# Kernel tuning notes

Measured on AMD Instinct MI355X. Metric: run time of the kernel, lower is better.

The kernel has to match this reference:

```python
import jax, jax.numpy as jnp
import numpy as np

N = 4096
DIM_IN = 512
DIM_Q = 128
DIM_K = 128
NUM_GRAPHS = 16
NODES_PER_GRAPH = N // NUM_GRAPHS
NEG = -1000000.0


def setup_inputs() -> dict:
    key = jax.random.key(0)
    ks = jax.random.split(key, 10)
    x = jax.random.normal(ks[0], (N, DIM_IN), dtype=jnp.float32)
    b = jax.random.normal(ks[1], (N, N), dtype=jnp.float32)
    c = jax.random.normal(ks[2], (N, N), dtype=jnp.float32)
    sparse_mask = jax.random.randint(ks[3], (N, N), 0, 2).astype(jnp.int32)
    ptr = (jnp.arange(NUM_GRAPHS + 1) * NODES_PER_GRAPH).astype(jnp.int32)
    # linear layer params (q, k, v): y = x @ W.T + bias
    Wq = jax.random.normal(ks[4], (DIM_Q, DIM_IN), dtype=jnp.float32) * 0.02
    bq = jnp.zeros((DIM_Q,), dtype=jnp.float32)
    Wk = jax.random.normal(ks[5], (DIM_K, DIM_IN), dtype=jnp.float32) * 0.02
    bk = jnp.zeros((DIM_K,), dtype=jnp.float32)
    Wv = jax.random.normal(ks[6], (DIM_K, DIM_IN), dtype=jnp.float32) * 0.02
    bv = jnp.zeros((DIM_K,), dtype=jnp.float32)
    return {"x": x, "b": b, "c": c, "ptr": ptr, "sparse_mask": sparse_mask,
            "Wq": Wq, "bq": bq, "Wk": Wk, "bk": bk, "Wv": Wv, "bv": bv}


def reference(x, b, c, ptr, sparse_mask, Wq, bq, Wk, bk, Wv, bv):
    n = x.shape[0]
    q = x @ Wq.T + bq            # [N, dq]
    k = x @ Wk.T + bk            # [N, dk]
    v = x @ Wv.T + bv            # [N, dk]
    # graph id per node from ptr; block-diagonal (same-graph) mask
    gid = jnp.searchsorted(ptr, jnp.arange(n), side='right') - 1
    block = gid[:, None] == gid[None, :]                       # [N, N] bool
    scale = q.shape[-1] ** 0.5
    # compute_a: QK^T/sqrt(dq) on the block diagonal, zeros elsewhere
    a = jnp.where(block, (q @ k.T) / scale, 0.0)
    a = a + b + c
    keep = block & (sparse_mask != 0)
    a = jnp.where(keep, a, NEG)
    sm = jax.nn.softmax(a, axis=-1) * keep.astype(x.dtype)
    return sm @ v
```

## Files before the change

### kernel.cpp

```cpp
#include <hip/hip_runtime.h>
#include <hip/hip_bf16.h>

#define N_NODES 4096
#define DIM_IN 512
#define DIM_QK 128
#define BLK 256
#define NUM_G 16
#define NEGV -1000000.0f

typedef __bf16 bf16x8 __attribute__((ext_vector_type(8)));
typedef float  f32x4  __attribute__((ext_vector_type(4)));

__global__ __launch_bounds__(256) void cvt_kernel(
    const float* __restrict__ x,
    const float* __restrict__ Wq, const float* __restrict__ Wk,
    const float* __restrict__ Wv,
    __bf16* __restrict__ xb, __bf16* __restrict__ wb)
{
    const int i = blockIdx.x * 256 + threadIdx.x;
    if (i < 524288) {
        const float4 v = ((const float4*)x)[i];
        __bf16* o = xb + i * 4;
        o[0] = (__bf16)v.x; o[1] = (__bf16)v.y;
        o[2] = (__bf16)v.z; o[3] = (__bf16)v.w;
    } else {
        const int j = i - 524288;
        if (j < 49152) {
            const int m = j / 16384;
            const float* W = (m == 0) ? Wq : (m == 1 ? Wk : Wv);
            const float4 v = ((const float4*)W)[j - m * 16384];
            __bf16* o = wb + j * 4;
            o[0] = (__bf16)v.x; o[1] = (__bf16)v.y;
            o[2] = (__bf16)v.z; o[3] = (__bf16)v.w;
        }
    }
}

__global__ __launch_bounds__(128) void qkv_mfma(
    const __bf16* __restrict__ xb, const __bf16* __restrict__ wb,
    const float* __restrict__ bq, const float* __restrict__ bk,
    const float* __restrict__ bv,
    __bf16* __restrict__ qb, __bf16* __restrict__ kb, __bf16* __restrict__ vtb)
{
    const int mat    = blockIdx.y >> 1;
    const int colOff = (blockIdx.y & 1) * 64;
    const int wave = threadIdx.x >> 6;
    const int lane = threadIdx.x & 63;
    const int lr   = lane & 15;
    const int quad = lane >> 4;
    const int row0 = blockIdx.x * 32 + wave * 16;

    const __bf16* W    = wb + mat * (DIM_QK * DIM_IN);
    const float*  bias = (mat == 0) ? bq : (mat == 1 ? bk : bv);

    f32x4 acc[4];
    #pragma unroll
    for (int i = 0; i < 4; ++i) acc[i] = (f32x4){0.f, 0.f, 0.f, 0.f};

    const __bf16* arow = xb + (size_t)(row0 + lr) * DIM_IN + quad * 8;
    const __bf16* brow = W + (size_t)(colOff + lr) * DIM_IN + quad * 8;

    #pragma unroll 4
    for (int kt = 0; kt < 16; ++kt) {
        const bf16x8 a = *(const bf16x8*)(arow + kt * 32);
        #pragma unroll
        for (int nt = 0; nt < 4; ++nt) {
            const bf16x8 b = *(const bf16x8*)(brow + nt * 16 * DIM_IN + kt * 32);
            acc[nt] = __builtin_amdgcn_mfma_f32_16x16x32_bf16(a, b, acc[nt], 0, 0, 0);
        }
    }

    #pragma unroll
    for (int nt = 0; nt < 4; ++nt) {
        const int col = colOff + nt * 16 + lr;
        const float bs = bias[col];
        #pragma unroll
        for (int r = 0; r < 4; ++r) {
            const int row = row0 + quad * 4 + r;
            const __bf16 o = (__bf16)(acc[nt][r] + bs);
            if (mat == 0)      qb[(size_t)row * DIM_QK + col] = o;
            else if (mat == 1) kb[(size_t)row * DIM_QK + col] = o;
            else               vtb[(size_t)col * N_NODES + row] = o;
        }
    }
}

#define PSTR 272

__global__ __launch_bounds__(256, 1) void attn_mfma(
    const float* __restrict__ bmat, const float* __restrict__ cmat,
    const int* __restrict__ mask,
    const __bf16* __restrict__ qb, const __bf16* __restrict__ kb,
    const __bf16* __restrict__ vtb,
    float* __restrict__ out)
{
    __shared__ __bf16 plds[16 * PSTR];
    __shared__ float redm[4][16];
    __shared__ float reds[4][16];

    const int tid  = threadIdx.x;
    const int w    = tid >> 6;
    const int lane = tid & 63;
    const int lr   = lane & 15;
    const int quad = lane >> 4;
    const int g    = blockIdx.x >> 4;
    const int tile = blockIdx.x & 15;
    const int row0 = g * BLK + tile * 16;
    const int col0 = g * BLK;

    bf16x8 aq[4];
    #pragma unroll
    for (int kt = 0; kt < 4; ++kt)
        aq[kt] = *(const bf16x8*)(qb + (size_t)(row0 + lr) * DIM_QK + kt * 32 + quad * 8);

    bf16x8 bk[16];
    #pragma unroll
    for (int kt = 0; kt < 4; ++kt)
        #pragma unroll
        for (int nt = 0; nt < 4; ++nt)
            bk[kt * 4 + nt] = *(const bf16x8*)(kb
                + (size_t)(col0 + w * 64 + nt * 16 + lr) * DIM_QK + kt * 32 + quad * 8);

    bf16x8 bv[16];
    #pragma unroll
    for (int nt2 = 0; nt2 < 2; ++nt2)
        #pragma unroll
        for (int kt = 0; kt < 8; ++kt)
            bv[nt2 * 8 + kt] = *(const bf16x8*)(vtb
                + (size_t)(w * 32 + nt2 * 16 + lr) * N_NODES + col0 + kt * 32 + quad * 8);

    float bbv[16], ccv[16];
    int   mmv[16];
    #pragma unroll
    for (int nt = 0; nt < 4; ++nt)
        #pragma unroll
        for (int r = 0; r < 4; ++r) {
            const size_t idx = (size_t)(row0 + quad * 4 + r) * N_NODES
                             + col0 + w * 64 + nt * 16 + lr;
            bbv[nt * 4 + r] = bmat[idx];
            ccv[nt * 4 + r] = cmat[idx];
            mmv[nt * 4 + r] = mask[idx];
        }

    f32x4 s[4];
    #pragma unroll
    for (int nt = 0; nt < 4; ++nt) s[nt] = (f32x4){0.f, 0.f, 0.f, 0.f};

    #pragma unroll
    for (int kt = 0; kt < 4; ++kt)
        #pragma unroll
        for (int nt = 0; nt < 4; ++nt)
            s[nt] = __builtin_amdgcn_mfma_f32_16x16x32_bf16(aq[kt], bk[kt * 4 + nt],
                                                            s[nt], 0, 0, 0);

    const float rscale = 0.08838834764831845f;
    #pragma unroll
    for (int nt = 0; nt < 4; ++nt)
        #pragma unroll
        for (int r = 0; r < 4; ++r) {
            const int i = nt * 4 + r;
            s[nt][r] = mmv[i] ? (s[nt][r] * rscale + bbv[i] + ccv[i]) : NEGV;
        }

    float mr[4] = {-3e38f, -3e38f, -3e38f, -3e38f};
    #pragma unroll
    for (int nt = 0; nt < 4; ++nt)
        #pragma unroll
        for (int r = 0; r < 4; ++r) mr[r] = fmaxf(mr[r], s[nt][r]);
    #pragma unroll
    for (int off = 1; off <= 8; off <<= 1)
        #pragma unroll
        for (int r = 0; r < 4; ++r) mr[r] = fmaxf(mr[r], __shfl_xor(mr[r], off));
    if (lr == 0) {
        #pragma unroll
        for (int r = 0; r < 4; ++r) redm[w][quad * 4 + r] = mr[r];
    }
    __syncthreads();
    float M[4];
    #pragma unroll
    for (int r = 0; r < 4; ++r) {
        const int rw = quad * 4 + r;
        M[r] = fmaxf(fmaxf(redm[0][rw], redm[1][rw]), fmaxf(redm[2][rw], redm[3][rw]));
    }

    float sum[4] = {0.f, 0.f, 0.f, 0.f};
    #pragma unroll
    for (int nt = 0; nt < 4; ++nt)
        #pragma unroll
        for (int r = 0; r < 4; ++r) {
            const float e = (s[nt][r] > -1e5f) ? __expf(s[nt][r] - M[r]) : 0.f;
            s[nt][r] = e;
            sum[r] += e;
        }
    #pragma unroll
    for (int off = 1; off <= 8; off <<= 1)
        #pragma unroll
        for (int r = 0; r < 4; ++r) sum[r] += __shfl_xor(sum[r], off);
    if (lr == 0) {
        #pragma unroll
        for (int r = 0; r < 4; ++r) reds[w][quad * 4 + r] = sum[r];
    }
    __syncthreads();
    float inv[4];
    #pragma unroll
    for (int r = 0; r < 4; ++r) {
        const int rw = quad * 4 + r;
        const float t = reds[0][rw] + reds[1][rw] + reds[2][rw] + reds[3][rw];
        inv[r] = (t > 0.f) ? (1.f / t) : 0.f;
    }

    #pragma unroll
    for (int nt = 0; nt < 4; ++nt)
        #pragma unroll
        for (int r = 0; r < 4; ++r)
            plds[(quad * 4 + r) * PSTR + w * 64 + nt * 16 + lr] =
                (__bf16)(s[nt][r] * inv[r]);
    __syncthreads();

    #pragma unroll
    for (int nt2 = 0; nt2 < 2; ++nt2) {
        f32x4 o = (f32x4){0.f, 0.f, 0.f, 0.f};
        #pragma unroll
        for (int kt = 0; kt < 8; ++kt) {
            const bf16x8 a = *(const bf16x8*)(plds + lr * PSTR + kt * 32 + quad * 8);
            o = __builtin_amdgcn_mfma_f32_16x16x32_bf16(a, bv[nt2 * 8 + kt], o, 0, 0, 0);
        }
        #pragma unroll
        for (int r = 0; r < 4; ++r)
            out[(size_t)(row0 + quad * 4 + r) * DIM_QK + w * 32 + nt2 * 16 + lr] = o[r];
    }
}

extern "C" void kernel_launch(void* const* d_in, const int* in_sizes, int n_in,
                              void* d_out, int out_size, void* d_ws, size_t ws_size,
                              hipStream_t stream) {
    const float* x    = (const float*)d_in[0];
    const float* bmat = (const float*)d_in[1];
    const float* cmat = (const float*)d_in[2];
    const int*   mask = (const int*)d_in[4];
    const float* Wq   = (const float*)d_in[5];
    const float* bq   = (const float*)d_in[6];
    const float* Wk   = (const float*)d_in[7];
    const float* bk   = (const float*)d_in[8];
    const float* Wv   = (const float*)d_in[9];
    const float* bv   = (const float*)d_in[10];
    float* out = (float*)d_out;

    __bf16* xb  = (__bf16*)d_ws;
    __bf16* wb  = xb + (size_t)N_NODES * DIM_IN;
    __bf16* qb  = wb + 3 * DIM_QK * DIM_IN;
    __bf16* kb  = qb + (size_t)N_NODES * DIM_QK;
    __bf16* vtb = kb + (size_t)N_NODES * DIM_QK;

    cvt_kernel<<<dim3((524288 + 49152 + 255) / 256), 256, 0, stream>>>(
        x, Wq, Wk, Wv, xb, wb);

    qkv_mfma<<<dim3(128, 6), 128, 0, stream>>>(
        xb, wb, bq, bk, bv, qb, kb, vtb);

    attn_mfma<<<dim3(NUM_G * 16), 256, 0, stream>>>(
        bmat, cmat, mask, qb, kb, vtb, out);
}
```

Measured before the change: 196.4 us.

## Fuse fp32-to-bf16 conversion into QKV projection and double rows per wave

Removes the separate conversion kernel and has the QKV projection read fp32 x and weights directly, converting to bf16 in registers before the MFMA. Each wave now computes two 16-row tiles sharing each weight fragment, which halves the grid and reuses the converted B operand. This saves one launch and the write and re-read of the bf16 copies of x and the weights. In exchange each block reads twice as many bytes of fp32 input and does the conversion arithmetic inline. Variables in the attention kernel are renamed without any functional change.

```diff
diff --git a/kernel.cpp b/kernel.cpp
--- a/kernel.cpp
+++ b/kernel.cpp
@@ -11,33 +11,19 @@
 typedef __bf16 bf16x8 __attribute__((ext_vector_type(8)));
 typedef float  f32x4  __attribute__((ext_vector_type(4)));
 
-__global__ __launch_bounds__(256) void cvt_kernel(
+__device__ __forceinline__ bf16x8 cvt8(const float* p) {
+    const float4 a = *(const float4*)p;
+    const float4 b = *(const float4*)(p + 4);
+    bf16x8 o;
+    o[0] = (__bf16)a.x; o[1] = (__bf16)a.y; o[2] = (__bf16)a.z; o[3] = (__bf16)a.w;
+    o[4] = (__bf16)b.x; o[5] = (__bf16)b.y; o[6] = (__bf16)b.z; o[7] = (__bf16)b.w;
+    return o;
+}
+
+__global__ __launch_bounds__(128) void qkv_mfma(
     const float* __restrict__ x,
     const float* __restrict__ Wq, const float* __restrict__ Wk,
     const float* __restrict__ Wv,
-    __bf16* __restrict__ xb, __bf16* __restrict__ wb)
-{
-    const int i = blockIdx.x * 256 + threadIdx.x;
-    if (i < 524288) {
-        const float4 v = ((const float4*)x)[i];
-        __bf16* o = xb + i * 4;
-        o[0] = (__bf16)v.x; o[1] = (__bf16)v.y;
-        o[2] = (__bf16)v.z; o[3] = (__bf16)v.w;
-    } else {
-        const int j = i - 524288;
-        if (j < 49152) {
-            const int m = j / 16384;
-            const float* W = (m == 0) ? Wq : (m == 1 ? Wk : Wv);
-            const float4 v = ((const float4*)W)[j - m * 16384];
-            __bf16* o = wb + j * 4;
-            o[0] = (__bf16)v.x; o[1] = (__bf16)v.y;
-            o[2] = (__bf16)v.z; o[3] = (__bf16)v.w;
-        }
-    }
-}
-
-__global__ __launch_bounds__(128) void qkv_mfma(
-    const __bf16* __restrict__ xb, const __bf16* __restrict__ wb,
     const float* __restrict__ bq, const float* __restrict__ bk,
     const float* __restrict__ bv,
     __bf16* __restrict__ qb, __bf16* __restrict__ kb, __bf16* __restrict__ vtb)
@@ -48,41 +34,48 @@
     const int lane = threadIdx.x & 63;
     const int lr   = lane & 15;
     const int quad = lane >> 4;
-    const int row0 = blockIdx.x * 32 + wave * 16;
-
-    const __bf16* W    = wb + mat * (DIM_QK * DIM_IN);
-    const float*  bias = (mat == 0) ? bq : (mat == 1 ? bk : bv);
-
-    f32x4 acc[4];
-    #pragma unroll
-    for (int i = 0; i < 4; ++i) acc[i] = (f32x4){0.f, 0.f, 0.f, 0.f};
-
-    const __bf16* arow = xb + (size_t)(row0 + lr) * DIM_IN + quad * 8;
-    const __bf16* brow = W + (size_t)(colOff + lr) * DIM_IN + quad * 8;
+    const int row0 = blockIdx.x * 64 + wave * 32;
+
+    const float* W    = (mat == 0) ? Wq : (mat == 1 ? Wk : Wv);
+    const float* bias = (mat == 0) ? bq : (mat == 1 ? bk : bv);
+
+    f32x4 acc[2][4];
+    #pragma unroll
+    for (int mt = 0; mt < 2; ++mt)
+        #pragma unroll
+        for (int nt = 0; nt < 4; ++nt) acc[mt][nt] = (f32x4){0.f, 0.f, 0.f, 0.f};
+
+    const float* arow0 = x + (size_t)(row0 + lr) * DIM_IN + quad * 8;
+    const float* arow1 = x + (size_t)(row0 + 16 + lr) * DIM_IN + quad * 8;
+    const float* brow  = W + (size_t)(colOff + lr) * DIM_IN + quad * 8;
 
     #pragma unroll 4
     for (int kt = 0; kt < 16; ++kt) {
-        const bf16x8 a = *(const bf16x8*)(arow + kt * 32);
+        const bf16x8 a0 = cvt8(arow0 + kt * 32);
+        const bf16x8 a1 = cvt8(arow1 + kt * 32);
         #pragma unroll
         for (int nt = 0; nt < 4; ++nt) {
-            const bf16x8 b = *(const bf16x8*)(brow + nt * 16 * DIM_IN + kt * 32);
-            acc[nt] = __builtin_amdgcn_mfma_f32_16x16x32_bf16(a, b, acc[nt], 0, 0, 0);
-        }
-    }
-
-    #pragma unroll
-    for (int nt = 0; nt < 4; ++nt) {
-        const int col = colOff + nt * 16 + lr;
-        const float bs = bias[col];
-        #pragma unroll
-        for (int r = 0; r < 4; ++r) {
-            const int row = row0 + quad * 4 + r;
-            const __bf16 o = (__bf16)(acc[nt][r] + bs);
-            if (mat == 0)      qb[(size_t)row * DIM_QK + col] = o;
-            else if (mat == 1) kb[(size_t)row * DIM_QK + col] = o;
-            else               vtb[(size_t)col * N_NODES + row] = o;
-        }
-    }
+            const bf16x8 b = cvt8(brow + nt * 16 * DIM_IN + kt * 32);
+            acc[0][nt] = __builtin_amdgcn_mfma_f32_16x16x32_bf16(a0, b, acc[0][nt], 0, 0, 0);
+            acc[1][nt] = __builtin_amdgcn_mfma_f32_16x16x32_bf16(a1, b, acc[1][nt], 0, 0, 0);
+        }
+    }
+
+    #pragma unroll
+    for (int mt = 0; mt < 2; ++mt)
+        #pragma unroll
+        for (int nt = 0; nt < 4; ++nt) {
+            const int col = colOff + nt * 16 + lr;
+            const float bs = bias[col];
+            #pragma unroll
+            for (int r = 0; r < 4; ++r) {
+                const int row = row0 + mt * 16 + quad * 4 + r;
+                const __bf16 o = (__bf16)(acc[mt][nt][r] + bs);
+                if (mat == 0)      qb[(size_t)row * DIM_QK + col] = o;
+                else if (mat == 1) kb[(size_t)row * DIM_QK + col] = o;
+                else               vtb[(size_t)col * N_NODES + row] = o;
+            }
+        }
 }
 
 #define PSTR 272
@@ -113,20 +106,20 @@
     for (int kt = 0; kt < 4; ++kt)
         aq[kt] = *(const bf16x8*)(qb + (size_t)(row0 + lr) * DIM_QK + kt * 32 + quad * 8);
 
-    bf16x8 bk[16];
+    bf16x8 bkf[16];
     #pragma unroll
     for (int kt = 0; kt < 4; ++kt)
         #pragma unroll
         for (int nt = 0; nt < 4; ++nt)
-            bk[kt * 4 + nt] = *(const bf16x8*)(kb
+            bkf[kt * 4 + nt] = *(const bf16x8*)(kb
                 + (size_t)(col0 + w * 64 + nt * 16 + lr) * DIM_QK + kt * 32 + quad * 8);
 
-    bf16x8 bv[16];
+    bf16x8 bvf[16];
     #pragma unroll
     for (int nt2 = 0; nt2 < 2; ++nt2)
         #pragma unroll
         for (int kt = 0; kt < 8; ++kt)
-            bv[nt2 * 8 + kt] = *(const bf16x8*)(vtb
+            bvf[nt2 * 8 + kt] = *(const bf16x8*)(vtb
                 + (size_t)(w * 32 + nt2 * 16 + lr) * N_NODES + col0 + kt * 32 + quad * 8);
 
     float bbv[16], ccv[16];
@@ -150,7 +143,7 @@
     for (int kt = 0; kt < 4; ++kt)
         #pragma unroll
         for (int nt = 0; nt < 4; ++nt)
-            s[nt] = __builtin_amdgcn_mfma_f32_16x16x32_bf16(aq[kt], bk[kt * 4 + nt],
+            s[nt] = __builtin_amdgcn_mfma_f32_16x16x32_bf16(aq[kt], bkf[kt * 4 + nt],
                                                             s[nt], 0, 0, 0);
 
     const float rscale = 0.08838834764831845f;
@@ -223,7 +216,7 @@
         #pragma unroll
         for (int kt = 0; kt < 8; ++kt) {
             const bf16x8 a = *(const bf16x8*)(plds + lr * PSTR + kt * 32 + quad * 8);
-            o = __builtin_amdgcn_mfma_f32_16x16x32_bf16(a, bv[nt2 * 8 + kt], o, 0, 0, 0);
+            o = __builtin_amdgcn_mfma_f32_16x16x32_bf16(a, bvf[nt2 * 8 + kt], o, 0, 0, 0);
         }
         #pragma unroll
         for (int r = 0; r < 4; ++r)
@@ -246,17 +239,12 @@
     const float* bv   = (const float*)d_in[10];
     float* out = (float*)d_out;
 
-    __bf16* xb  = (__bf16*)d_ws;
-    __bf16* wb  = xb + (size_t)N_NODES * DIM_IN;
-    __bf16* qb  = wb + 3 * DIM_QK * DIM_IN;
+    __bf16* qb  = (__bf16*)d_ws;
     __bf16* kb  = qb + (size_t)N_NODES * DIM_QK;
     __bf16* vtb = kb + (size_t)N_NODES * DIM_QK;
 
-    cvt_kernel<<<dim3((524288 + 49152 + 255) / 256), 256, 0, stream>>>(
-        x, Wq, Wk, Wv, xb, wb);
-
-    qkv_mfma<<<dim3(128, 6), 128, 0, stream>>>(
-        xb, wb, bq, bk, bv, qb, kb, vtb);
+    qkv_mfma<<<dim3(64, 6), 128, 0, stream>>>(
+        x, Wq, Wk, Wv, bq, bk, bv, qb, kb, vtb);
 
     attn_mfma<<<dim3(NUM_G * 16), 256, 0, stream>>>(
         bmat, cmat, mask, qb, kb, vtb, out);
```

Result: slower. 222.7 us (+13.4%).
